# Performance work log

Hardware: AMD Instinct MI355X
Metric: run time of the kernel (lower is better)

Reference implementation:

```python
import jax, jax.numpy as jnp
import numpy as np

N_SITES = 64
BOND = 128
BATCH = 16384


def _mid_bond_shapes(n, bd):
    # Reproduces the bond-dimension schedule in MPS.__init__ for the N-2 middle sites.
    shapes = []
    for imx in range(n // 2):
        if imx == 0:
            continue  # first site is [2, 2]
        l, r = 2 ** imx, 2 ** (imx + 1)
        if l <= bd and r >= bd:
            r = bd
        elif l >= bd and r >= bd:
            l, r = bd, bd
        shapes.append((l, r))
    for imx in range(n // 2, n):
        if imx == n - 1:
            continue  # last site is [2, 2]
        r, l = 2 ** (n - 1 - imx), 2 ** (n - imx)
        if l >= bd and r >= bd:
            l, r = bd, bd
        elif l >= bd and r <= bd:
            l = bd
        shapes.append((l, r))
    return shapes


def setup_inputs() -> dict:
    key = jax.random.key(0)
    k1, k2, k3 = jax.random.split(key, 3)
    x = jax.random.normal(k1, (BATCH, N_SITES, 2), dtype=jnp.float32)
    scale = (2.0 * BOND) ** -0.5  # keeps the 62-step chain numerically stable
    # Middle site tensors, zero-padded into a uniform [N-2, D, 2, D] stack.
    rng = np.random.default_rng(0)
    w_mid = np.zeros((N_SITES - 2, BOND, 2, BOND), dtype=np.float32)
    for k, (l, r) in enumerate(_mid_bond_shapes(N_SITES, BOND)):
        w_mid[k, :l, :, :r] = rng.normal(0.0, scale, size=(l, 2, r)).astype(np.float32)
    w_first = scale * jax.random.normal(k2, (2, 2), dtype=jnp.float32)  # [i, r]
    w_last = scale * jax.random.normal(k3, (2, 2), dtype=jnp.float32)   # [l, i]
    return {"x": x, "w_first": w_first, "w_mid": jnp.asarray(w_mid), "w_last": w_last}


def reference(x, w_first, w_mid, w_last):
    # x: [B, N, 2] pre-embedded input (embed_input passes 3D input through unchanged).
    D = w_mid.shape[1]
    # Site 0: 'ir,bi->br'
    v = jnp.einsum("ir,bi->br", w_first, x[:, 0])          # [B, 2]
    v = jnp.pad(v, ((0, 0), (0, D - v.shape[1])))           # [B, D], zero-padded
    xm = jnp.swapaxes(x[:, 1:-1], 0, 1)                     # [N-2, B, 2]

    def step(v, wx):
        W, xk = wx  # W: [D, 2, D], xk: [B, 2]
        # Fuses the per-site 'lir,bi->blr' einsum with the sequential bmm chain:
        # v_new[b, r] = sum_{l,i} v[b, l] * W[l, i, r] * x[b, i]
        return jnp.einsum("bl,lir,bi->br", v, W, xk), None

    v, _ = jax.lax.scan(step, v, (w_mid, xm))               # [B, D]
    # Last site: 'li,bi->bl' then contract with the chain state (valid bond = 2).
    out = jnp.einsum("bl,li,bi->b", v[:, :2], w_last, x[:, -1])
    return out[:, None]                                     # [B, 1], matches squeeze(tem, 2)
```

## Files before the change

kernel.cpp:

```cpp
#include <hip/hip_runtime.h>
#include <stdint.h>

#define NMID  62
#define NPAIR 31
#define NBATCH 16384
#define BT    64

typedef __attribute__((ext_vector_type(8))) _Float16 half8;
typedef __attribute__((ext_vector_type(4))) float f32x4;
typedef __attribute__((ext_vector_type(4))) unsigned int u32x4;
typedef __attribute__((ext_vector_type(2))) unsigned int u32x2;

__device__ __forceinline__ unsigned short f16_bits(float f) {
    _Float16 h = (_Float16)f;
    return __builtin_bit_cast(unsigned short, h);
}

__device__ __forceinline__ float g_scale(int k) {
    int rk = (k < 5) ? (4 << k) : ((k < 56) ? 128 : (64 >> (k - 56)));
    return 16.0f * rsqrtf((float)rk);
}

__global__ __launch_bounds__(256) void mps_pack_w2(
    const float* __restrict__ wm, unsigned* __restrict__ wpk)
{
    __shared__ float Bs[128][16];
    const int tr  = blockIdx.x & 7;
    const int i12 = (blockIdx.x >> 3) & 3;
    const int p   = blockIdx.x >> 5;
    const int i1 = i12 >> 1, i2 = i12 & 1;
    const int tid = threadIdx.x, lane = tid & 63, wv = tid >> 6;
    const int arow = lane & 15, ag = lane >> 4;
    const float* A  = wm + ((size_t)(2 * p) * 128) * 256 + i1 * 128;
    const float* Bm = wm + ((size_t)(2 * p + 1) * 128) * 256 + i2 * 128;

    for (int idx = tid; idx < 128 * 16; idx += 256) {
        int m = idx >> 4, rr = idx & 15;
        Bs[m][rr] = Bm[(size_t)m * 256 + tr * 16 + rr];
    }
    __syncthreads();

    half8 bf[4];
    #pragma unroll
    for (int mk = 0; mk < 4; ++mk) {
        half8 h;
        #pragma unroll
        for (int j = 0; j < 8; ++j)
            h[j] = (_Float16)Bs[mk * 32 + ag * 8 + j][arow];
        bf[mk] = h;
    }
    #pragma unroll
    for (int tll = 0; tll < 2; ++tll) {
        const int tl = wv * 2 + tll;
        f32x4 acc = f32x4{0.f, 0.f, 0.f, 0.f};
        #pragma unroll
        for (int mk = 0; mk < 4; ++mk) {
            const float* ap = A + (size_t)(tl * 16 + arow) * 256 + mk * 32 + ag * 8;
            float4 a0 = *reinterpret_cast<const float4*>(ap);
            float4 a1 = *reinterpret_cast<const float4*>(ap + 4);
            half8 ah;
            ah[0] = (_Float16)a0.x; ah[1] = (_Float16)a0.y;
            ah[2] = (_Float16)a0.z; ah[3] = (_Float16)a0.w;
            ah[4] = (_Float16)a1.x; ah[5] = (_Float16)a1.y;
            ah[6] = (_Float16)a1.z; ah[7] = (_Float16)a1.w;
            acc = __builtin_amdgcn_mfma_f32_16x16x32_f16(ah, bf[mk], acc, 0, 0, 0);
        }
        const int l0 = tl * 16 + ag * 4;
        const int kt = l0 >> 5;
        const int o = l0 & 31;
        const int agf = o >> 3;
        const int d0 = (o & 7) >> 1;
        unsigned w0 = (unsigned)f16_bits(acc[0]) | ((unsigned)f16_bits(acc[1]) << 16);
        unsigned w1 = (unsigned)f16_bits(acc[2]) | ((unsigned)f16_bits(acc[3]) << 16);
        size_t dw = ((((size_t)(p * 4 + i12) * 8 + tr) * 4 + kt) * 64
                     + (agf * 16 + arow)) * 4 + d0;
        *reinterpret_cast<u32x2*>(wpk + dw) = u32x2{w0, w1};
    }
}

__device__ __forceinline__ void rd_vf(const unsigned short* __restrict__ vcur,
                                      int kt, int arow, int ag, half8 (&vf)[4]) {
    #pragma unroll
    for (int bt = 0; bt < 4; ++bt) {
        int row = bt * 16 + arow;
        int boff = (row * 256 + kt * 64 + ag * 16) ^ ((row & 7) << 4);
        vf[bt] = *reinterpret_cast<const half8*>(
            reinterpret_cast<const char*>(vcur) + boff);
    }
}
__device__ __forceinline__ void mm_kt(f32x4 (&acc)[4][4], const u32x4 (&W)[16],
                                      const half8 (&vf)[4], int kt) {
    #pragma unroll
    for (int bt = 0; bt < 4; ++bt)
        #pragma unroll
        for (int i12 = 0; i12 < 4; ++i12)
            acc[bt][i12] = __builtin_amdgcn_mfma_f32_16x16x32_f16(
                __builtin_bit_cast(half8, W[i12 * 4 + kt]), vf[bt],
                acc[bt][i12], 0, 0, 0);
}

__device__ __forceinline__ void do_pair(
    int p, const float* __restrict__ Pt, int lane, int rt,
    const unsigned short* __restrict__ vcur, unsigned short* __restrict__ vnxt,
    const u32x4* __restrict__ wpk, int pnext,
    u32x4 (&Wcur)[16], u32x4 (&Wnxt)[16])
{
    const int arow = lane & 15, ag = lane >> 4;

    #pragma unroll
    for (int j = 0; j < 16; ++j)
        asm volatile("" : "+v"(Wcur[j]));

    #pragma unroll
    for (int i12 = 0; i12 < 4; ++i12)
        #pragma unroll
        for (int kt = 0; kt < 4; ++kt)
            Wnxt[i12 * 4 + kt] =
                wpk[(((size_t)(pnext * 4 + i12) * 8 + rt) * 4 + kt) * 64 + lane];

    f32x4 Pv[4];
    #pragma unroll
    for (int bt = 0; bt < 4; ++bt)
        Pv[bt] = *reinterpret_cast<const f32x4*>(&Pt[(p * 64 + bt * 16 + arow) * 4]);

    f32x4 acc[4][4];
    #pragma unroll
    for (int bt = 0; bt < 4; ++bt)
        #pragma unroll
        for (int i12 = 0; i12 < 4; ++i12)
            acc[bt][i12] = f32x4{0.f, 0.f, 0.f, 0.f};

    half8 v0[4], v1[4];
    rd_vf(vcur, 0, arow, ag, v0);
    rd_vf(vcur, 1, arow, ag, v1);
    mm_kt(acc, Wcur, v0, 0);
    rd_vf(vcur, 2, arow, ag, v0);
    mm_kt(acc, Wcur, v1, 1);
    rd_vf(vcur, 3, arow, ag, v1);
    mm_kt(acc, Wcur, v0, 2);
    mm_kt(acc, Wcur, v1, 3);

    #pragma unroll
    for (int bt = 0; bt < 4; ++bt) {
        unsigned short h[4];
        #pragma unroll
        for (int q = 0; q < 4; ++q) {
            float vn = Pv[bt][0] * acc[bt][0][q] + Pv[bt][1] * acc[bt][1][q]
                     + Pv[bt][2] * acc[bt][2][q] + Pv[bt][3] * acc[bt][3][q];
            h[q] = f16_bits(vn);
        }
        int row = bt * 16 + arow;
        int byte = (row * 256 + (rt * 16 + ag * 4) * 2) ^ ((row & 7) << 4);
        u32x2 pk;
        pk[0] = (unsigned)h[0] | ((unsigned)h[1] << 16);
        pk[1] = (unsigned)h[2] | ((unsigned)h[3] << 16);
        *reinterpret_cast<u32x2*>(reinterpret_cast<char*>(vnxt) + byte) = pk;
    }
    __syncthreads();
}

__global__ __launch_bounds__(512, 2) void mps_mfma(
    const float* __restrict__ x, const float* __restrict__ wf,
    const float* __restrict__ wl, const u32x4* __restrict__ wpk,
    float* __restrict__ out)
{
    __shared__ unsigned short vh0[BT * 128];
    __shared__ unsigned short vh1[BT * 128];
    __shared__ float Pt[NPAIR * BT * 4];
    const int tid = threadIdx.x;
    const int lane = tid & 63;
    const int rt = tid >> 6;
    const int bbase = blockIdx.x * BT;

    for (int idx = tid; idx < NPAIR * BT; idx += 512) {
        int pp = idx >> 6, row = idx & 63;
        const float* xb = &x[(size_t)(bbase + row) * 128 + 2 + 4 * pp];
        float2 xa = *reinterpret_cast<const float2*>(xb);
        float2 xc = *reinterpret_cast<const float2*>(xb + 2);
        float n2a = fmaf(xa.x, xa.x, fmaf(xa.y, xa.y, 1e-30f));
        float n2b = fmaf(xc.x, xc.x, fmaf(xc.y, xc.y, 1e-30f));
        float s = g_scale(2 * pp) * rsqrtf(n2a) * g_scale(2 * pp + 1) * rsqrtf(n2b);
        Pt[idx * 4 + 0] = s * xa.x * xc.x;
        Pt[idx * 4 + 1] = s * xa.x * xc.y;
        Pt[idx * 4 + 2] = s * xa.y * xc.x;
        Pt[idx * 4 + 3] = s * xa.y * xc.y;
    }

    const float wf00 = wf[0], wf01 = wf[1], wf10 = wf[2], wf11 = wf[3];
    for (int idx = tid; idx < BT * 128; idx += 512) {
        int row = idx >> 7, l = idx & 127;
        float val = 0.f;
        if (l < 2) {
            float x0 = x[(size_t)(bbase + row) * 128 + 0];
            float x1 = x[(size_t)(bbase + row) * 128 + 1];
            float n2 = fmaf(x0, x0, fmaf(x1, x1, 1e-30f));
            float si = 8.0f * rsqrtf(n2);
            val = si * ((l == 0) ? (wf00 * x0 + wf10 * x1) : (wf01 * x0 + wf11 * x1));
        }
        int byte = (row * 256 + l * 2) ^ ((row & 7) << 4);
        *reinterpret_cast<unsigned short*>(
            reinterpret_cast<char*>(vh0) + byte) = f16_bits(val);
    }
    __syncthreads();

    u32x4 WA[16], WB[16];
    #pragma unroll
    for (int i12 = 0; i12 < 4; ++i12)
        #pragma unroll
        for (int kt = 0; kt < 4; ++kt)
            WA[i12 * 4 + kt] = wpk[(((size_t)i12 * 8 + rt) * 4 + kt) * 64 + lane];

    for (int p = 0; p < 30; p += 2) {
        do_pair(p,     Pt, lane, rt, vh0, vh1, wpk, p + 1, WA, WB);
        do_pair(p + 1, Pt, lane, rt, vh1, vh0, wpk, p + 2, WB, WA);
    }
    do_pair(30, Pt, lane, rt, vh0, vh1, wpk, 30, WA, WB);

    if (tid < BT) {
        int row = tid;
        const float* xb = &x[(size_t)(bbase + row) * 128];
        float n2i = fmaf(xb[0], xb[0], fmaf(xb[1], xb[1], 1e-30f));
        float alpha = 8.0f * rsqrtf(n2i);
        for (int k = 0; k < NMID; ++k) {
            float2 xx = *reinterpret_cast<const float2*>(&xb[2 + 2 * k]);
            float n2 = fmaf(xx.x, xx.x, fmaf(xx.y, xx.y, 1e-30f));
            alpha *= g_scale(k) * rsqrtf(n2);
        }
        int boff = (row * 256) ^ ((row & 7) << 4);
        unsigned hw = *reinterpret_cast<unsigned*>(
            reinterpret_cast<char*>(vh1) + boff);
        float v0 = (float)__builtin_bit_cast(_Float16, (unsigned short)(hw & 0xffffu));
        float v1 = (float)__builtin_bit_cast(_Float16, (unsigned short)(hw >> 16));
        float x0 = xb[126], x1 = xb[127];
        float val = v0 * (wl[0] * x0 + wl[1] * x1)
                  + v1 * (wl[2] * x0 + wl[3] * x1);
        out[bbase + row] = val / alpha;
    }
}

#define FBT 32
__global__ __launch_bounds__(256, 2) void mps_chain_kernel(
    const float* __restrict__ x, const float* __restrict__ wf,
    const float* __restrict__ wm, const float* __restrict__ wl,
    float* __restrict__ out)
{
    __shared__ float vbuf[2][128][FBT];
    __shared__ float xs_lds[FBT][126];
    const int tid = threadIdx.x;
    const int rg = tid >> 3, bg = tid & 7;
    const int r0 = rg * 4, b0 = bg * 4;
    const int bbase = blockIdx.x * FBT;
    for (int idx = tid; idx < FBT * 126; idx += 256) {
        int b = idx / 126, j = idx % 126;
        xs_lds[b][j] = x[(size_t)(bbase + b) * 128 + 2 + j];
    }
    const float wf00 = wf[0], wf01 = wf[1], wf10 = wf[2], wf11 = wf[3];
    for (int idx = tid; idx < 128 * FBT; idx += 256) {
        int l = idx / FBT, b = idx % FBT;
        float val = 0.0f;
        if (l < 2) {
            float x0 = x[(size_t)(bbase + b) * 128 + 0];
            float x1 = x[(size_t)(bbase + b) * 128 + 1];
            val = (l == 0) ? (wf00 * x0 + wf10 * x1) : (wf01 * x0 + wf11 * x1);
        }
        vbuf[0][l][b] = val;
    }
    __syncthreads();
    int cur = 0;
    for (int k = 0; k < NMID; ++k) {
        const float* __restrict__ Wk = wm + (size_t)k * (2 * 128 * 128);
        float acc0[4][4], acc1[4][4];
        #pragma unroll
        for (int bb = 0; bb < 4; ++bb)
            #pragma unroll
            for (int rr = 0; rr < 4; ++rr) { acc0[bb][rr] = 0.0f; acc1[bb][rr] = 0.0f; }
        #pragma unroll 4
        for (int l = 0; l < 128; ++l) {
            float4 vv = *reinterpret_cast<const float4*>(&vbuf[cur][l][b0]);
            float4 w0 = *reinterpret_cast<const float4*>(&Wk[(size_t)(2 * l) * 128 + r0]);
            float4 w1 = *reinterpret_cast<const float4*>(&Wk[(size_t)(2 * l + 1) * 128 + r0]);
            float va[4] = { vv.x, vv.y, vv.z, vv.w };
            float w0a[4] = { w0.x, w0.y, w0.z, w0.w };
            float w1a[4] = { w1.x, w1.y, w1.z, w1.w };
            #pragma unroll
            for (int bb = 0; bb < 4; ++bb)
                #pragma unroll
                for (int rr = 0; rr < 4; ++rr) {
                    acc0[bb][rr] = fmaf(va[bb], w0a[rr], acc0[bb][rr]);
                    acc1[bb][rr] = fmaf(va[bb], w1a[rr], acc1[bb][rr]);
                }
        }
        const int nxt = cur ^ 1;
        float vn[4][4];
        #pragma unroll
        for (int bb = 0; bb < 4; ++bb) {
            float xx0 = xs_lds[b0 + bb][2 * k + 0];
            float xx1 = xs_lds[b0 + bb][2 * k + 1];
            #pragma unroll
            for (int rr = 0; rr < 4; ++rr)
                vn[bb][rr] = xx0 * acc0[bb][rr] + xx1 * acc1[bb][rr];
        }
        #pragma unroll
        for (int rr = 0; rr < 4; ++rr) {
            float4 wv = make_float4(vn[0][rr], vn[1][rr], vn[2][rr], vn[3][rr]);
            *reinterpret_cast<float4*>(&vbuf[nxt][r0 + rr][b0]) = wv;
        }
        cur = nxt;
        __syncthreads();
    }
    if (rg == 0) {
        const float wl00 = wl[0], wl01 = wl[1], wl10 = wl[2], wl11 = wl[3];
        #pragma unroll
        for (int bb = 0; bb < 4; ++bb) {
            int b = b0 + bb;
            float v0 = vbuf[cur][0][b];
            float v1 = vbuf[cur][1][b];
            float xx0 = xs_lds[b][124];
            float xx1 = xs_lds[b][125];
            out[bbase + b] = v0 * (wl00 * xx0 + wl01 * xx1)
                           + v1 * (wl10 * xx0 + wl11 * xx1);
        }
    }
}

extern "C" void kernel_launch(void* const* d_in, const int* in_sizes, int n_in,
                              void* d_out, int out_size, void* d_ws, size_t ws_size,
                              hipStream_t stream) {
    const float* x  = (const float*)d_in[0];
    const float* wf = (const float*)d_in[1];
    const float* wm = (const float*)d_in[2];
    const float* wl = (const float*)d_in[3];
    float* out = (float*)d_out;

    const size_t ws_needed = (size_t)NPAIR * 4 * 8 * 4 * 64 * 16;
    if (ws_size >= ws_needed) {
        hipLaunchKernelGGL(mps_pack_w2, dim3(NPAIR * 4 * 8), dim3(256), 0, stream,
                           wm, (unsigned*)d_ws);
        hipLaunchKernelGGL(mps_mfma, dim3(NBATCH / BT), dim3(512), 0, stream,
                           x, wf, wl, (const u32x4*)d_ws, out);
    } else {
        hipLaunchKernelGGL(mps_chain_kernel, dim3(NBATCH / FBT), dim3(256), 0, stream,
                           x, wf, wm, wl, out);
    }
}
```

Before: 88.10 us.

## Halve batch tile and drop weight double-buffering to raise occupancy

Reduces the per-block batch tile from 64 to 32 rows, drops the register double-buffered prefetch of the next pair's packed weights in favour of loading weights at the start of each pair, and raises launch bounds to 4 blocks per CU. Fewer accumulators and weight registers per thread should allow more resident waves to hide latency. In exchange, each block reloads the full weight set for half as many rows, doubling weight traffic per row, and the weight load latency is no longer overlapped with the previous pair's compute.

```diff
diff --git a/kernel.cpp b/kernel.cpp
--- a/kernel.cpp
+++ b/kernel.cpp
@@ -4,7 +4,7 @@
 #define NMID  62
 #define NPAIR 31
 #define NBATCH 16384
-#define BT    64
+#define BT    32
 
 typedef __attribute__((ext_vector_type(8))) _Float16 half8;
 typedef __attribute__((ext_vector_type(4))) float f32x4;
@@ -78,70 +78,54 @@
     }
 }
 
-__device__ __forceinline__ void rd_vf(const unsigned short* __restrict__ vcur,
-                                      int kt, int arow, int ag, half8 (&vf)[4]) {
-    #pragma unroll
-    for (int bt = 0; bt < 4; ++bt) {
-        int row = bt * 16 + arow;
-        int boff = (row * 256 + kt * 64 + ag * 16) ^ ((row & 7) << 4);
-        vf[bt] = *reinterpret_cast<const half8*>(
-            reinterpret_cast<const char*>(vcur) + boff);
-    }
-}
-__device__ __forceinline__ void mm_kt(f32x4 (&acc)[4][4], const u32x4 (&W)[16],
-                                      const half8 (&vf)[4], int kt) {
-    #pragma unroll
-    for (int bt = 0; bt < 4; ++bt)
-        #pragma unroll
-        for (int i12 = 0; i12 < 4; ++i12)
-            acc[bt][i12] = __builtin_amdgcn_mfma_f32_16x16x32_f16(
-                __builtin_bit_cast(half8, W[i12 * 4 + kt]), vf[bt],
-                acc[bt][i12], 0, 0, 0);
-}
-
 __device__ __forceinline__ void do_pair(
     int p, const float* __restrict__ Pt, int lane, int rt,
     const unsigned short* __restrict__ vcur, unsigned short* __restrict__ vnxt,
-    const u32x4* __restrict__ wpk, int pnext,
-    u32x4 (&Wcur)[16], u32x4 (&Wnxt)[16])
+    const u32x4* __restrict__ wpk)
 {
     const int arow = lane & 15, ag = lane >> 4;
 
-    #pragma unroll
-    for (int j = 0; j < 16; ++j)
-        asm volatile("" : "+v"(Wcur[j]));
-
+    u32x4 W[16];
     #pragma unroll
     for (int i12 = 0; i12 < 4; ++i12)
         #pragma unroll
         for (int kt = 0; kt < 4; ++kt)
-            Wnxt[i12 * 4 + kt] =
-                wpk[(((size_t)(pnext * 4 + i12) * 8 + rt) * 4 + kt) * 64 + lane];
-
-    f32x4 Pv[4];
-    #pragma unroll
-    for (int bt = 0; bt < 4; ++bt)
-        Pv[bt] = *reinterpret_cast<const f32x4*>(&Pt[(p * 64 + bt * 16 + arow) * 4]);
-
-    f32x4 acc[4][4];
-    #pragma unroll
-    for (int bt = 0; bt < 4; ++bt)
+            W[i12 * 4 + kt] =
+                wpk[(((size_t)(p * 4 + i12) * 8 + rt) * 4 + kt) * 64 + lane];
+
+    f32x4 Pv[2];
+    #pragma unroll
+    for (int bt = 0; bt < 2; ++bt)
+        Pv[bt] = *reinterpret_cast<const f32x4*>(&Pt[(p * BT + bt * 16 + arow) * 4]);
+
+    f32x4 acc[2][4];
+    #pragma unroll
+    for (int bt = 0; bt < 2; ++bt)
         #pragma unroll
         for (int i12 = 0; i12 < 4; ++i12)
             acc[bt][i12] = f32x4{0.f, 0.f, 0.f, 0.f};
 
-    half8 v0[4], v1[4];
-    rd_vf(vcur, 0, arow, ag, v0);
-    rd_vf(vcur, 1, arow, ag, v1);
-    mm_kt(acc, Wcur, v0, 0);
-    rd_vf(vcur, 2, arow, ag, v0);
-    mm_kt(acc, Wcur, v1, 1);
-    rd_vf(vcur, 3, arow, ag, v1);
-    mm_kt(acc, Wcur, v0, 2);
-    mm_kt(acc, Wcur, v1, 3);
-
-    #pragma unroll
-    for (int bt = 0; bt < 4; ++bt) {
+    #pragma unroll
+    for (int kt = 0; kt < 4; ++kt) {
+        half8 vf[2];
+        #pragma unroll
+        for (int bt = 0; bt < 2; ++bt) {
+            int row = bt * 16 + arow;
+            int boff = (row * 256 + kt * 64 + ag * 16) ^ ((row & 7) << 4);
+            vf[bt] = *reinterpret_cast<const half8*>(
+                reinterpret_cast<const char*>(vcur) + boff);
+        }
+        #pragma unroll
+        for (int bt = 0; bt < 2; ++bt)
+            #pragma unroll
+            for (int i12 = 0; i12 < 4; ++i12)
+                acc[bt][i12] = __builtin_amdgcn_mfma_f32_16x16x32_f16(
+                    __builtin_bit_cast(half8, W[i12 * 4 + kt]), vf[bt],
+                    acc[bt][i12], 0, 0, 0);
+    }
+
+    #pragma unroll
+    for (int bt = 0; bt < 2; ++bt) {
         unsigned short h[4];
         #pragma unroll
         for (int q = 0; q < 4; ++q) {
@@ -159,7 +143,7 @@
     __syncthreads();
 }
 
-__global__ __launch_bounds__(512, 2) void mps_mfma(
+__global__ __launch_bounds__(512, 4) void mps_mfma(
     const float* __restrict__ x, const float* __restrict__ wf,
     const float* __restrict__ wl, const u32x4* __restrict__ wpk,
     float* __restrict__ out)
@@ -173,7 +157,7 @@
     const int bbase = blockIdx.x * BT;
 
     for (int idx = tid; idx < NPAIR * BT; idx += 512) {
-        int pp = idx >> 6, row = idx & 63;
+        int pp = idx / BT, row = idx % BT;
         const float* xb = &x[(size_t)(bbase + row) * 128 + 2 + 4 * pp];
         float2 xa = *reinterpret_cast<const float2*>(xb);
         float2 xc = *reinterpret_cast<const float2*>(xb + 2);
@@ -203,18 +187,11 @@
     }
     __syncthreads();
 
-    u32x4 WA[16], WB[16];
-    #pragma unroll
-    for (int i12 = 0; i12 < 4; ++i12)
-        #pragma unroll
-        for (int kt = 0; kt < 4; ++kt)
-            WA[i12 * 4 + kt] = wpk[(((size_t)i12 * 8 + rt) * 4 + kt) * 64 + lane];
-
     for (int p = 0; p < 30; p += 2) {
-        do_pair(p,     Pt, lane, rt, vh0, vh1, wpk, p + 1, WA, WB);
-        do_pair(p + 1, Pt, lane, rt, vh1, vh0, wpk, p + 2, WB, WA);
-    }
-    do_pair(30, Pt, lane, rt, vh0, vh1, wpk, 30, WA, WB);
+        do_pair(p,     Pt, lane, rt, vh0, vh1, wpk);
+        do_pair(p + 1, Pt, lane, rt, vh1, vh0, wpk);
+    }
+    do_pair(30, Pt, lane, rt, vh0, vh1, wpk);
 
     if (tid < BT) {
         int row = tid;
```

After: 108.6 us. +23.3%, slower.
